# Kernel tuning notes

Hardware: AMD Instinct MI355X
Metric: run time of the kernel (lower is better)

The kernel has to match this reference:

```python
import jax, jax.numpy as jnp
import numpy as np

B, D, E = 8192, 4096, 64
TOP_K = 2
NOISE_EPSILON = 0.01


def setup_inputs() -> dict:
    key = jax.random.key(0)
    k1, k2, k3, k4 = jax.random.split(key, 4)
    return {
        "x": jax.random.normal(k1, (B, D), dtype=jnp.float32),
        # nn.Linear weights, init std=0.1, no bias; torch stores [out, in]
        "gate_w": jax.random.normal(k2, (E, D), dtype=jnp.float32) * 0.1,
        "noise_gate_w": jax.random.normal(k3, (E, D), dtype=jnp.float32) * 0.1,
        # deterministic stand-in for torch.randn_like(clean_logits)
        "noise": jax.random.normal(k4, (B, E), dtype=jnp.float32),
    }


def reference(x, gate_w, noise_gate_w, noise):
    # clean_logits = x @ W_g^T : [B, E]
    clean_logits = jnp.einsum("bd,ed->be", x, gate_w)
    # training path: noisy logits with softplus-scaled noise
    noise_logits = jnp.einsum("bd,ed->be", x, noise_gate_w)
    noisy_logits = clean_logits + noise * jax.nn.softplus(noise_logits) * NOISE_EPSILON
    # top-k over experts, softmax over the k selected logits
    top_k_logits, top_k_indices = jax.lax.top_k(noisy_logits, TOP_K)  # [B, k]
    top_k_gates = jax.nn.softmax(top_k_logits, axis=-1)
    # scatter back into dense [B, E] gates
    rows = jnp.arange(noisy_logits.shape[0])[:, None]  # [B, 1]
    gates = jnp.zeros_like(noisy_logits).at[rows, top_k_indices].set(top_k_gates)
    load = jax.nn.softmax(clean_logits, axis=-1)
    return (gates, load)
```

## Files before the change

### kernel.cpp

```cpp
#include <hip/hip_runtime.h>
#include <math.h>

#define BB 8192
#define DD 4096
#define EE 64

constexpr float NOISE_EPS = 0.01f;
constexpr int BM = 64;

typedef __attribute__((ext_vector_type(8))) _Float16 f16x8;
typedef __attribute__((ext_vector_type(4))) float    f32x4;

__device__ __forceinline__ void split8(const float4& a, const float4& b,
                                       f16x8& hi, f16x8& mi) {
    float v[8] = {a.x, a.y, a.z, a.w, b.x, b.y, b.z, b.w};
    #pragma unroll
    for (int j = 0; j < 8; ++j) {
        _Float16 h = (_Float16)v[j];
        hi[j] = h;
        mi[j] = (_Float16)(v[j] - (float)h);
    }
}

__global__ __launch_bounds__(256) void wsplit_pack(
    const float* __restrict__ gw, const float* __restrict__ ngw,
    char* __restrict__ wpk)
{
    const int gid = blockIdx.x * 256 + threadIdx.x;
    const int r   = gid >> 9;
    const int kc  = gid & 511;
    const int k0  = kc * 8;
    const float* src = (r < EE) ? gw + (size_t)r * DD + k0
                                : ngw + (size_t)(r - EE) * DD + k0;
    float4 a = *reinterpret_cast<const float4*>(src);
    float4 b = *reinterpret_cast<const float4*>(src + 4);
    f16x8 hi, mi;
    split8(a, b, hi, mi);
    const int T    = k0 >> 5;
    const int kq   = (k0 >> 3) & 3;
    const int cb   = r >> 4;
    const int lane = kq * 16 + (r & 15);
    char* base = wpk + (size_t)T * 16384;
    *reinterpret_cast<f16x8*>(base + ((cb * 2 + 0) * 64 + lane) * 16) = hi;
    *reinterpret_cast<f16x8*>(base + ((cb * 2 + 1) * 64 + lane) * 16) = mi;
}

template <int SK>
__global__ __launch_bounds__(512, 4) void gating_main(
    const float* __restrict__ x,
    const char*  __restrict__ wpk,
    float* __restrict__ partial)
{
    constexpr int KC   = DD / SK;
    constexpr int NKS  = KC / 64;
    constexpr int GMAX = 2 * NKS - 1;

    __shared__ __align__(1024) char xls[2][16384];

    const int tid  = threadIdx.x;
    const int bid  = blockIdx.x;
    const int sk   = bid & (SK - 1);
    const int row0 = (bid / SK) * BM;
    const int lane = tid & 63;
    const int n8   = tid >> 6;
    const int l15  = lane & 15;
    const int kq   = lane >> 4;

    const int sr = tid >> 3;
    const int sj = tid & 7;
    const float* xg = x + (size_t)(row0 + sr) * DD + sk * KC + sj * 8;
    const int wo0 = sr * 256 + 0 * 128 + ((sj ^ (sr & 7)) << 4);
    const int wo1 = sr * 256 + 1 * 128 + ((sj ^ (sr & 7)) << 4);

    int rbase[4], swz[4];
    #pragma unroll
    for (int ms = 0; ms < 4; ++ms) {
        const int r = ms * 16 + l15;
        rbase[ms] = r * 256;
        swz[ms]   = r & 7;
    }

    const char* wpkB = wpk + ((size_t)(sk * NKS * 2) << 14) + lane * 16;
    const int oh = (2 * n8 + 0) * 1024;
    const int om = (2 * n8 + 1) * 1024;

    f32x4 acc0 = {0.f,0.f,0.f,0.f}, acc1 = {0.f,0.f,0.f,0.f};
    f32x4 acc2 = {0.f,0.f,0.f,0.f}, acc3 = {0.f,0.f,0.f,0.f};

    #define LOADB(g, H, M) do {                                                \
        const char* _b = wpkB + ((size_t)(g) << 14);                           \
        H = *reinterpret_cast<const f16x8*>(_b + oh);                          \
        M = *reinterpret_cast<const f16x8*>(_b + om);                          \
    } while (0)

    #define CHUNK(bufp, gc, H, M) do {                                         \
        const char* _xb = (bufp);                                              \
        const int _c = (gc) & 1;                                               \
        f16x8 ah0 = *reinterpret_cast<const f16x8*>(_xb + rbase[0] +           \
                        ((((_c << 2) | kq) ^ swz[0]) << 4));                   \
        f16x8 am0 = *reinterpret_cast<const f16x8*>(_xb + rbase[0] + 128 +     \
                        ((((_c << 2) | kq) ^ swz[0]) << 4));                   \
        f16x8 ah1 = *reinterpret_cast<const f16x8*>(_xb + rbase[1] +           \
                        ((((_c << 2) | kq) ^ swz[1]) << 4));                   \
        f16x8 am1 = *reinterpret_cast<const f16x8*>(_xb + rbase[1] + 128 +     \
                        ((((_c << 2) | kq) ^ swz[1]) << 4));                   \
        f16x8 ah2 = *reinterpret_cast<const f16x8*>(_xb + rbase[2] +           \
                        ((((_c << 2) | kq) ^ swz[2]) << 4));                   \
        f16x8 am2 = *reinterpret_cast<const f16x8*>(_xb + rbase[2] + 128 +     \
                        ((((_c << 2) | kq) ^ swz[2]) << 4));                   \
        f16x8 ah3 = *reinterpret_cast<const f16x8*>(_xb + rbase[3] +           \
                        ((((_c << 2) | kq) ^ swz[3]) << 4));                   \
        f16x8 am3 = *reinterpret_cast<const f16x8*>(_xb + rbase[3] + 128 +     \
                        ((((_c << 2) | kq) ^ swz[3]) << 4));                   \
        acc0 = __builtin_amdgcn_mfma_f32_16x16x32_f16(ah0, H, acc0, 0,0,0);    \
        acc1 = __builtin_amdgcn_mfma_f32_16x16x32_f16(ah1, H, acc1, 0,0,0);    \
        acc2 = __builtin_amdgcn_mfma_f32_16x16x32_f16(ah2, H, acc2, 0,0,0);    \
        acc3 = __builtin_amdgcn_mfma_f32_16x16x32_f16(ah3, H, acc3, 0,0,0);    \
        acc0 = __builtin_amdgcn_mfma_f32_16x16x32_f16(am0, H, acc0, 0,0,0);    \
        acc1 = __builtin_amdgcn_mfma_f32_16x16x32_f16(am1, H, acc1, 0,0,0);    \
        acc2 = __builtin_amdgcn_mfma_f32_16x16x32_f16(am2, H, acc2, 0,0,0);    \
        acc3 = __builtin_amdgcn_mfma_f32_16x16x32_f16(am3, H, acc3, 0,0,0);    \
        acc0 = __builtin_amdgcn_mfma_f32_16x16x32_f16(ah0, M, acc0, 0,0,0);    \
        acc1 = __builtin_amdgcn_mfma_f32_16x16x32_f16(ah1, M, acc1, 0,0,0);    \
        acc2 = __builtin_amdgcn_mfma_f32_16x16x32_f16(ah2, M, acc2, 0,0,0);    \
        acc3 = __builtin_amdgcn_mfma_f32_16x16x32_f16(ah3, M, acc3, 0,0,0);    \
        { const int _g = (gc) + 2;                                             \
          LOADB((_g <= GMAX) ? _g : GMAX, H, M); }                             \
    } while (0)

    #define WSPLIT(bp, V0, V1) do {                                            \
        f16x8 _hi, _mi;                                                        \
        split8(V0, V1, _hi, _mi);                                              \
        *reinterpret_cast<f16x8*>((bp) + wo0) = _hi;                           \
        *reinterpret_cast<f16x8*>((bp) + wo1) = _mi;                           \
    } while (0)

    char* buf0 = (char*)xls[0];
    char* buf1 = (char*)xls[1];

    float4 xA0, xA1, xB0, xB1;
    f16x8 pH, pM, qH, qM;

    xA0 = *reinterpret_cast<const float4*>(xg);
    xA1 = *reinterpret_cast<const float4*>(xg + 4);
    xB0 = *reinterpret_cast<const float4*>(xg + 64);
    xB1 = *reinterpret_cast<const float4*>(xg + 64 + 4);
    WSPLIT(buf0, xA0, xA1);
    LOADB(0, pH, pM);
    LOADB(1, qH, qM);

    for (int t = 0; t < NKS; t += 2) {
        asm volatile("s_waitcnt lgkmcnt(0)" ::: "memory");
        __builtin_amdgcn_s_barrier();
        if (t + 2 < NKS) {
            xA0 = *reinterpret_cast<const float4*>(xg + (size_t)(t + 2) * 64);
            xA1 = *reinterpret_cast<const float4*>(xg + (size_t)(t + 2) * 64 + 4);
        }
        WSPLIT(buf1, xB0, xB1);
        CHUNK(buf0, 2 * t,     pH, pM);
        CHUNK(buf0, 2 * t + 1, qH, qM);

        asm volatile("s_waitcnt lgkmcnt(0)" ::: "memory");
        __builtin_amdgcn_s_barrier();
        if (t + 3 < NKS) {
            xB0 = *reinterpret_cast<const float4*>(xg + (size_t)(t + 3) * 64);
            xB1 = *reinterpret_cast<const float4*>(xg + (size_t)(t + 3) * 64 + 4);
        }
        if (t + 2 < NKS) WSPLIT(buf0, xA0, xA1);
        CHUNK(buf1, 2 * t + 2, pH, pM);
        CHUNK(buf1, 2 * t + 3, qH, qM);
    }

    #undef LOADB
    #undef CHUNK
    #undef WSPLIT

    const size_t pbase = ((size_t)sk * BB + row0) * 128;
    #pragma unroll
    for (int ms = 0; ms < 4; ++ms) {
        f32x4 a = (ms == 0) ? acc0 : (ms == 1) ? acc1 : (ms == 2) ? acc2 : acc3;
        #pragma unroll
        for (int j = 0; j < 4; ++j) {
            const int r = ms * 16 + kq * 4 + j;
            const int c = n8 * 16 + l15;
            partial[pbase + (size_t)r * 128 + c] = a[j];
        }
    }
}

template <int SK>
__global__ __launch_bounds__(512) void gating_epi(
    const float* __restrict__ partial,
    const float* __restrict__ noise,
    float* __restrict__ out)
{
    const int tid  = threadIdx.x;
    const int wv   = tid >> 6;
    const int lane = tid & 63;
    const int l15  = lane & 15;
    const int kq   = lane >> 4;
    const int grow = blockIdx.x * 32 + wv * 4 + kq;
    const int s    = l15;

    const float* pb = partial + (size_t)grow * 128 + 4 * s;
    float4 c4 = {0.f,0.f,0.f,0.f}, n4 = {0.f,0.f,0.f,0.f};
    #pragma unroll
    for (int k = 0; k < SK; ++k) {
        const float* p = pb + (size_t)k * BB * 128;
        float4 a = *reinterpret_cast<const float4*>(p);
        float4 b = *reinterpret_cast<const float4*>(p + 64);
        c4.x += a.x; c4.y += a.y; c4.z += a.z; c4.w += a.w;
        n4.x += b.x; n4.y += b.y; n4.z += b.z; n4.w += b.w;
    }

    float4 nz = *reinterpret_cast<const float4*>(noise + (size_t)grow * EE + 4 * s);

    float cc[4] = {c4.x, c4.y, c4.z, c4.w};
    float nl[4] = {n4.x, n4.y, n4.z, n4.w};
    float m1 = -3.4e38f, m2 = -3.4e38f;
    int   i1 = -1, i2 = -1;
    float cmax = -3.4e38f;
    #pragma unroll
    for (int j = 0; j < 4; ++j) {
        const int e = 4 * s + j;
        float sp  = fmaxf(nl[j], 0.0f) + log1pf(expf(-fabsf(nl[j])));
        float nzj = (j == 0) ? nz.x : (j == 1) ? nz.y : (j == 2) ? nz.z : nz.w;
        float vno = fmaf(nzj * sp, NOISE_EPS, cc[j]);
        if (vno > m1)      { m2 = m1; i2 = i1; m1 = vno; i1 = e; }
        else if (vno > m2) { m2 = vno; i2 = e; }
        cmax = fmaxf(cmax, cc[j]);
    }

    #pragma unroll
    for (int m = 1; m < 16; m <<= 1) {
        float b1 = __shfl_xor(m1, m, 16);
        int  bi1 = __shfl_xor(i1, m, 16);
        float b2 = __shfl_xor(m2, m, 16);
        int  bi2 = __shfl_xor(i2, m, 16);
        cmax = fmaxf(cmax, __shfl_xor(cmax, m, 16));

        bool bwin = (b1 > m1) || (b1 == m1 && bi1 < i1);
        float t1; int ti1; float t2; int ti2;
        if (bwin) {
            t1 = b1; ti1 = bi1;
            bool aw = (m1 > b2) || (m1 == b2 && i1 < bi2);
            t2 = aw ? m1 : b2; ti2 = aw ? i1 : bi2;
        } else {
            t1 = m1; ti1 = i1;
            bool bw = (b1 > m2) || (b1 == m2 && bi1 < i2);
            t2 = bw ? b1 : m2; ti2 = bw ? bi1 : i2;
        }
        m1 = t1; i1 = ti1; m2 = t2; i2 = ti2;
    }

    float tq = expf(m2 - m1);
    float p1 = 1.0f / (1.0f + tq);
    float p2 = tq * p1;

    float e0 = expf(cc[0] - cmax);
    float e1 = expf(cc[1] - cmax);
    float e2 = expf(cc[2] - cmax);
    float e3 = expf(cc[3] - cmax);
    float sum = e0 + e1 + e2 + e3;
    #pragma unroll
    for (int m = 1; m < 16; m <<= 1) sum += __shfl_xor(sum, m, 16);
    float inv = 1.0f / sum;

    const int eb = 4 * s;
    float4 gt;
    gt.x = (eb     == i1) ? p1 : (eb     == i2) ? p2 : 0.0f;
    gt.y = (eb + 1 == i1) ? p1 : (eb + 1 == i2) ? p2 : 0.0f;
    gt.z = (eb + 2 == i1) ? p1 : (eb + 2 == i2) ? p2 : 0.0f;
    gt.w = (eb + 3 == i1) ? p1 : (eb + 3 == i2) ? p2 : 0.0f;
    float4 ld = {e0 * inv, e1 * inv, e2 * inv, e3 * inv};

    *reinterpret_cast<float4*>(out + (size_t)grow * EE + eb) = gt;
    *reinterpret_cast<float4*>(out + (size_t)BB * EE + (size_t)grow * EE + eb) = ld;
}

extern "C" void kernel_launch(void* const* d_in, const int* in_sizes, int n_in,
                              void* d_out, int out_size, void* d_ws, size_t ws_size,
                              hipStream_t stream) {
    const float* x     = (const float*)d_in[0];
    const float* gw    = (const float*)d_in[1];
    const float* ngw   = (const float*)d_in[2];
    const float* noise = (const float*)d_in[3];
    float* out = (float*)d_out;

    char*  wpk     = (char*)d_ws;
    float* partial = (float*)(wpk + (size_t)2 * 1024 * 1024);

    const size_t MB = 1024 * 1024;

    hipLaunchKernelGGL(wsplit_pack, dim3(256), dim3(256), 0, stream, gw, ngw, wpk);

    if (ws_size >= 18 * MB) {
        hipLaunchKernelGGL(gating_main<4>, dim3((BB / BM) * 4), dim3(512), 0, stream,
                           x, wpk, partial);
        hipLaunchKernelGGL(gating_epi<4>, dim3(BB / 32), dim3(512), 0, stream,
                           partial, noise, out);
    } else if (ws_size >= 10 * MB) {
        hipLaunchKernelGGL(gating_main<2>, dim3((BB / BM) * 2), dim3(512), 0, stream,
                           x, wpk, partial);
        hipLaunchKernelGGL(gating_epi<2>, dim3(BB / 32), dim3(512), 0, stream,
                           partial, noise, out);
    } else {
        hipLaunchKernelGGL(gating_main<1>, dim3(BB / BM), dim3(512), 0, stream,
                           x, wpk, partial);
        hipLaunchKernelGGL(gating_epi<1>, dim3(BB / 32), dim3(512), 0, stream,
                           partial, noise, out);
    }
}
```

Baseline: 49.69 us.

## Warp-specialize gating GEMM into producer and MFMA consumer wavefronts

Splits the 8 wavefronts into 4 producers that load x from global memory, split it into fp16 hi/lo and write it to LDS, and 4 consumers that only load packed weights and issue MFMAs. Each consumer now covers two 16-column N tiles, doubling its accumulators and the weight registers it holds. The intent is to separate global-load and conversion latency from the MFMA stream. The cost is that half the waves do no matrix math, and consumers carry more register pressure under the 512,4 launch bounds.

```diff
diff --git a/kernel.cpp b/kernel.cpp
--- a/kernel.cpp
+++ b/kernel.cpp
@@ -62,16 +62,43 @@
     const int sk   = bid & (SK - 1);
     const int row0 = (bid / SK) * BM;
     const int lane = tid & 63;
-    const int n8   = tid >> 6;
+    const int wv   = tid >> 6;
+    const bool producer = (wv < 4);
     const int l15  = lane & 15;
     const int kq   = lane >> 4;
 
-    const int sr = tid >> 3;
-    const int sj = tid & 7;
-    const float* xg = x + (size_t)(row0 + sr) * DD + sk * KC + sj * 8;
-    const int wo0 = sr * 256 + 0 * 128 + ((sj ^ (sr & 7)) << 4);
-    const int wo1 = sr * 256 + 1 * 128 + ((sj ^ (sr & 7)) << 4);
-
+    char* buf0 = (char*)xls[0];
+    char* buf1 = (char*)xls[1];
+
+    const int pr = tid >> 2;
+    const int ps = tid & 3;
+    const float* xg = x + (size_t)(row0 + pr) * DD + sk * KC + ps * 16;
+    const int swp   = pr & 7;
+    const int wb    = pr * 256;
+    const int wo_h0 = wb       + (((2 * ps)     ^ swp) << 4);
+    const int wo_m0 = wb + 128 + (((2 * ps)     ^ swp) << 4);
+    const int wo_h1 = wb       + (((2 * ps + 1) ^ swp) << 4);
+    const int wo_m1 = wb + 128 + (((2 * ps + 1) ^ swp) << 4);
+
+    #define LOADX(t, V0, V1, V2, V3) do {                                      \
+        const float* _s = xg + (size_t)(t) * 64;                               \
+        V0 = *reinterpret_cast<const float4*>(_s);                             \
+        V1 = *reinterpret_cast<const float4*>(_s + 4);                         \
+        V2 = *reinterpret_cast<const float4*>(_s + 8);                         \
+        V3 = *reinterpret_cast<const float4*>(_s + 12);                        \
+    } while (0)
+
+    #define WSPLIT(bp, V0, V1, V2, V3) do {                                    \
+        f16x8 _h, _m;                                                          \
+        split8(V0, V1, _h, _m);                                                \
+        *reinterpret_cast<f16x8*>((bp) + wo_h0) = _h;                          \
+        *reinterpret_cast<f16x8*>((bp) + wo_m0) = _m;                          \
+        split8(V2, V3, _h, _m);                                                \
+        *reinterpret_cast<f16x8*>((bp) + wo_h1) = _h;                          \
+        *reinterpret_cast<f16x8*>((bp) + wo_m1) = _m;                          \
+    } while (0)
+
+    const int cw = wv - 4;
     int rbase[4], swz[4];
     #pragma unroll
     for (int ms = 0; ms < 4; ++ms) {
@@ -79,111 +106,107 @@
         rbase[ms] = r * 256;
         swz[ms]   = r & 7;
     }
-
-    const char* wpkB = wpk + ((size_t)(sk * NKS * 2) << 14) + lane * 16;
-    const int oh = (2 * n8 + 0) * 1024;
-    const int om = (2 * n8 + 1) * 1024;
-
-    f32x4 acc0 = {0.f,0.f,0.f,0.f}, acc1 = {0.f,0.f,0.f,0.f};
-    f32x4 acc2 = {0.f,0.f,0.f,0.f}, acc3 = {0.f,0.f,0.f,0.f};
-
-    #define LOADB(g, H, M) do {                                                \
+    const char* wpkB = wpk + ((size_t)(sk * NKS * 2) << 14)
+                           + ((cw & 3) * 4096) + lane * 16;
+
+    f32x4 acc[4][2];
+    #pragma unroll
+    for (int ms = 0; ms < 4; ++ms) {
+        acc[ms][0] = {0.f, 0.f, 0.f, 0.f};
+        acc[ms][1] = {0.f, 0.f, 0.f, 0.f};
+    }
+
+    #define LOADB(g, H0, M0, H1, M1) do {                                      \
         const char* _b = wpkB + ((size_t)(g) << 14);                           \
-        H = *reinterpret_cast<const f16x8*>(_b + oh);                          \
-        M = *reinterpret_cast<const f16x8*>(_b + om);                          \
+        H0 = *reinterpret_cast<const f16x8*>(_b);                              \
+        M0 = *reinterpret_cast<const f16x8*>(_b + 1024);                       \
+        H1 = *reinterpret_cast<const f16x8*>(_b + 2048);                       \
+        M1 = *reinterpret_cast<const f16x8*>(_b + 3072);                       \
     } while (0)
 
-    #define CHUNK(bufp, gc, H, M) do {                                         \
+    #define CHUNK(bufp, gc, H0, M0, H1, M1) do {                               \
         const char* _xb = (bufp);                                              \
         const int _c = (gc) & 1;                                               \
-        f16x8 ah0 = *reinterpret_cast<const f16x8*>(_xb + rbase[0] +           \
-                        ((((_c << 2) | kq) ^ swz[0]) << 4));                   \
-        f16x8 am0 = *reinterpret_cast<const f16x8*>(_xb + rbase[0] + 128 +     \
-                        ((((_c << 2) | kq) ^ swz[0]) << 4));                   \
-        f16x8 ah1 = *reinterpret_cast<const f16x8*>(_xb + rbase[1] +           \
-                        ((((_c << 2) | kq) ^ swz[1]) << 4));                   \
-        f16x8 am1 = *reinterpret_cast<const f16x8*>(_xb + rbase[1] + 128 +     \
-                        ((((_c << 2) | kq) ^ swz[1]) << 4));                   \
-        f16x8 ah2 = *reinterpret_cast<const f16x8*>(_xb + rbase[2] +           \
-                        ((((_c << 2) | kq) ^ swz[2]) << 4));                   \
-        f16x8 am2 = *reinterpret_cast<const f16x8*>(_xb + rbase[2] + 128 +     \
-                        ((((_c << 2) | kq) ^ swz[2]) << 4));                   \
-        f16x8 ah3 = *reinterpret_cast<const f16x8*>(_xb + rbase[3] +           \
-                        ((((_c << 2) | kq) ^ swz[3]) << 4));                   \
-        f16x8 am3 = *reinterpret_cast<const f16x8*>(_xb + rbase[3] + 128 +     \
-                        ((((_c << 2) | kq) ^ swz[3]) << 4));                   \
-        acc0 = __builtin_amdgcn_mfma_f32_16x16x32_f16(ah0, H, acc0, 0,0,0);    \
-        acc1 = __builtin_amdgcn_mfma_f32_16x16x32_f16(ah1, H, acc1, 0,0,0);    \
-        acc2 = __builtin_amdgcn_mfma_f32_16x16x32_f16(ah2, H, acc2, 0,0,0);    \
-        acc3 = __builtin_amdgcn_mfma_f32_16x16x32_f16(ah3, H, acc3, 0,0,0);    \
-        acc0 = __builtin_amdgcn_mfma_f32_16x16x32_f16(am0, H, acc0, 0,0,0);    \
-        acc1 = __builtin_amdgcn_mfma_f32_16x16x32_f16(am1, H, acc1, 0,0,0);    \
-        acc2 = __builtin_amdgcn_mfma_f32_16x16x32_f16(am2, H, acc2, 0,0,0);    \
-        acc3 = __builtin_amdgcn_mfma_f32_16x16x32_f16(am3, H, acc3, 0,0,0);    \
-        acc0 = __builtin_amdgcn_mfma_f32_16x16x32_f16(ah0, M, acc0, 0,0,0);    \
-        acc1 = __builtin_amdgcn_mfma_f32_16x16x32_f16(ah1, M, acc1, 0,0,0);    \
-        acc2 = __builtin_amdgcn_mfma_f32_16x16x32_f16(ah2, M, acc2, 0,0,0);    \
-        acc3 = __builtin_amdgcn_mfma_f32_16x16x32_f16(ah3, M, acc3, 0,0,0);    \
+        f16x8 ah[4], am[4];                                                    \
+        _Pragma("unroll")                                                      \
+        for (int ms = 0; ms < 4; ++ms) {                                       \
+            const int so = (((_c << 2) | kq) ^ swz[ms]) << 4;                  \
+            ah[ms] = *reinterpret_cast<const f16x8*>(_xb + rbase[ms] + so);    \
+            am[ms] = *reinterpret_cast<const f16x8*>(_xb + rbase[ms] + 128 + so);\
+        }                                                                      \
+        _Pragma("unroll")                                                      \
+        for (int ms = 0; ms < 4; ++ms) {                                       \
+            acc[ms][0] = __builtin_amdgcn_mfma_f32_16x16x32_f16(ah[ms], H0, acc[ms][0], 0,0,0); \
+            acc[ms][1] = __builtin_amdgcn_mfma_f32_16x16x32_f16(ah[ms], H1, acc[ms][1], 0,0,0); \
+        }                                                                      \
+        _Pragma("unroll")                                                      \
+        for (int ms = 0; ms < 4; ++ms) {                                       \
+            acc[ms][0] = __builtin_amdgcn_mfma_f32_16x16x32_f16(am[ms], H0, acc[ms][0], 0,0,0); \
+            acc[ms][1] = __builtin_amdgcn_mfma_f32_16x16x32_f16(am[ms], H1, acc[ms][1], 0,0,0); \
+        }                                                                      \
+        _Pragma("unroll")                                                      \
+        for (int ms = 0; ms < 4; ++ms) {                                       \
+            acc[ms][0] = __builtin_amdgcn_mfma_f32_16x16x32_f16(ah[ms], M0, acc[ms][0], 0,0,0); \
+            acc[ms][1] = __builtin_amdgcn_mfma_f32_16x16x32_f16(ah[ms], M1, acc[ms][1], 0,0,0); \
+        }                                                                      \
         { const int _g = (gc) + 2;                                             \
-          LOADB((_g <= GMAX) ? _g : GMAX, H, M); }                             \
+          LOADB((_g <= GMAX) ? _g : GMAX, H0, M0, H1, M1); }                   \
     } while (0)
 
-    #define WSPLIT(bp, V0, V1) do {                                            \
-        f16x8 _hi, _mi;                                                        \
-        split8(V0, V1, _hi, _mi);                                              \
-        *reinterpret_cast<f16x8*>((bp) + wo0) = _hi;                           \
-        *reinterpret_cast<f16x8*>((bp) + wo1) = _mi;                           \
-    } while (0)
-
-    char* buf0 = (char*)xls[0];
-    char* buf1 = (char*)xls[1];
-
-    float4 xA0, xA1, xB0, xB1;
-    f16x8 pH, pM, qH, qM;
-
-    xA0 = *reinterpret_cast<const float4*>(xg);
-    xA1 = *reinterpret_cast<const float4*>(xg + 4);
-    xB0 = *reinterpret_cast<const float4*>(xg + 64);
-    xB1 = *reinterpret_cast<const float4*>(xg + 64 + 4);
-    WSPLIT(buf0, xA0, xA1);
-    LOADB(0, pH, pM);
-    LOADB(1, qH, qM);
+    float4 xa0, xa1, xa2, xa3;
+    float4 xb0, xb1, xb2, xb3;
+    f16x8 pH0, pM0, pH1, pM1;
+    f16x8 qH0, qM0, qH1, qM1;
+
+    if (producer) {
+        LOADX(0, xa0, xa1, xa2, xa3);
+        WSPLIT(buf0, xa0, xa1, xa2, xa3);
+        LOADX(1, xb0, xb1, xb2, xb3);
+    } else {
+        LOADB(0, pH0, pM0, pH1, pM1);
+        LOADB(1, qH0, qM0, qH1, qM1);
+    }
 
     for (int t = 0; t < NKS; t += 2) {
         asm volatile("s_waitcnt lgkmcnt(0)" ::: "memory");
         __builtin_amdgcn_s_barrier();
-        if (t + 2 < NKS) {
-            xA0 = *reinterpret_cast<const float4*>(xg + (size_t)(t + 2) * 64);
-            xA1 = *reinterpret_cast<const float4*>(xg + (size_t)(t + 2) * 64 + 4);
+        if (producer) {
+            if (t + 2 < NKS) LOADX(t + 2, xa0, xa1, xa2, xa3);
+            WSPLIT(buf1, xb0, xb1, xb2, xb3);
+        } else {
+            CHUNK(buf0, 2 * t,     pH0, pM0, pH1, pM1);
+            CHUNK(buf0, 2 * t + 1, qH0, qM0, qH1, qM1);
         }
-        WSPLIT(buf1, xB0, xB1);
-        CHUNK(buf0, 2 * t,     pH, pM);
-        CHUNK(buf0, 2 * t + 1, qH, qM);
 
         asm volatile("s_waitcnt lgkmcnt(0)" ::: "memory");
         __builtin_amdgcn_s_barrier();
-        if (t + 3 < NKS) {
-            xB0 = *reinterpret_cast<const float4*>(xg + (size_t)(t + 3) * 64);
-            xB1 = *reinterpret_cast<const float4*>(xg + (size_t)(t + 3) * 64 + 4);
+        if (producer) {
+            if (t + 3 < NKS) LOADX(t + 3, xb0, xb1, xb2, xb3);
+            if (t + 2 < NKS) WSPLIT(buf0, xa0, xa1, xa2, xa3);
+        } else {
+            CHUNK(buf1, 2 * t + 2, pH0, pM0, pH1, pM1);
+            CHUNK(buf1, 2 * t + 3, qH0, qM0, qH1, qM1);
         }
-        if (t + 2 < NKS) WSPLIT(buf0, xA0, xA1);
-        CHUNK(buf1, 2 * t + 2, pH, pM);
-        CHUNK(buf1, 2 * t + 3, qH, qM);
-    }
-
+    }
+
+    #undef LOADX
+    #undef WSPLIT
     #undef LOADB
     #undef CHUNK
-    #undef WSPLIT
-
-    const size_t pbase = ((size_t)sk * BB + row0) * 128;
-    #pragma unroll
-    for (int ms = 0; ms < 4; ++ms) {
-        f32x4 a = (ms == 0) ? acc0 : (ms == 1) ? acc1 : (ms == 2) ? acc2 : acc3;
+
+    if (!producer) {
+        const size_t pbase = ((size_t)sk * BB + row0) * 128;
         #pragma unroll
-        for (int j = 0; j < 4; ++j) {
-            const int r = ms * 16 + kq * 4 + j;
-            const int c = n8 * 16 + l15;
-            partial[pbase + (size_t)r * 128 + c] = a[j];
+        for (int ms = 0; ms < 4; ++ms) {
+            #pragma unroll
+            for (int cb = 0; cb < 2; ++cb) {
+                #pragma unroll
+                for (int j = 0; j < 4; ++j) {
+                    const int r = ms * 16 + kq * 4 + j;
+                    const int c = (2 * cw + cb) * 16 + l15;
+                    partial[pbase + (size_t)r * 128 + c] = acc[ms][cb][j];
+                }
+            }
         }
     }
 }
```

New measurement: 49.15 us. About the same (-1.1%).
